# Optimization experiments

Hardware: AMD Instinct MI355X
Metric: run time of the kernel (lower is better)

The kernel has to match this reference:

```python
import jax, jax.numpy as jnp
import numpy as np

EMBED = 1024
HEADS = 16
HEAD_DIM = EMBED // HEADS
WINDOW = 256  # half-window = 128 on each side
B, S = 2, 2048


def setup_inputs() -> dict:
    key = jax.random.key(0)
    ks = jax.random.split(key, 9)
    std = 1.0 / np.sqrt(EMBED)
    def lin(k):
        kw, kb = jax.random.split(k)
        W = jax.random.uniform(kw, (EMBED, EMBED), jnp.float32, -std, std)
        b = jax.random.uniform(kb, (EMBED,), jnp.float32, -std, std)
        return W, b
    Wq, bq = lin(ks[0])
    Wk, bk = lin(ks[1])
    Wv, bv = lin(ks[2])
    Wo, bo = lin(ks[3])
    x = jax.random.normal(ks[4], (B, S, EMBED), jnp.float32)
    return {"x": x, "Wq": Wq, "bq": bq, "Wk": Wk, "bk": bk,
            "Wv": Wv, "bv": bv, "Wo": Wo, "bo": bo}


def reference(x, Wq, bq, Wk, bk, Wv, bv, Wo, bo):
    b, s, e = x.shape
    h, d = HEADS, HEAD_DIM
    # torch nn.Linear: y = x @ W.T + b
    def proj(W, bias):
        y = jnp.einsum('bse,fe->bsf', x, W) + bias
        return y.reshape(b, s, h, d).transpose(0, 2, 1, 3)  # [b,h,s,d]
    Q = proj(Wq, bq)
    K = proj(Wk, bk)
    V = proj(Wv, bv)
    # local mask: row i attends to cols [i - W//2, i + W//2] inclusive
    idx = jnp.arange(s)
    local_mask = jnp.abs(idx[:, None] - idx[None, :]) <= (WINDOW // 2)  # [s,s] bool
    scores = jnp.einsum('bhqd,bhkd->bhqk', Q, K) / jnp.sqrt(jnp.float32(d))
    scores = jnp.where(local_mask, scores, jnp.float32(-1e9))
    attn = jax.nn.softmax(scores, axis=-1)  # dropout is identity at eval
    out = jnp.einsum('bhqk,bhkd->bhqd', attn, V)
    out = out.transpose(0, 2, 1, 3).reshape(b, s, e)
    output = jnp.einsum('bse,fe->bsf', out, Wo) + bo
    return (output, attn)
```

## Files before the change

kernel.cpp:

```cpp
#include <hip/hip_runtime.h>
#include <hip/hip_bf16.h>
#include <stdint.h>

#define EMBED 1024
#define HEADS 16
#define HDIM 64
#define SEQ 2048
#define BATCH 2
#define MTOT (BATCH*SEQ)
#define KDIM EMBED
#define HALFW 128

typedef __attribute__((ext_vector_type(8))) short short8;
typedef __attribute__((ext_vector_type(4))) float floatx4;

__device__ __forceinline__ ushort f2bf(float f){
  uint32_t x = __float_as_uint(f);
  x += 0x7fffu + ((x >> 16) & 1u);
  return (ushort)(x >> 16);
}

__device__ __forceinline__ void gload16(const ushort* g, ushort* l){
  __builtin_amdgcn_global_load_lds(
      (__attribute__((address_space(1))) void*)(void*)g,
      (__attribute__((address_space(3))) void*)l, 16, 0, 0);
}

__global__ void cast_all(const float* __restrict__ x,  ushort* __restrict__ xb,
                         const float* __restrict__ Wq, const float* __restrict__ Wk,
                         const float* __restrict__ Wv, ushort* __restrict__ wqkv,
                         const float* __restrict__ Wo, ushort* __restrict__ wo)
{
  int bid = blockIdx.x;
  const float* src; ushort* dst; int base;
  if (bid < 4096){ src = x;  dst = xb;   base = bid; }
  else {
    int seg = (bid - 4096) >> 10;
    int sb  = (bid - 4096) & 1023;
    base = sb;
    if      (seg == 0){ src = Wq; dst = wqkv;           }
    else if (seg == 1){ src = Wk; dst = wqkv + 1048576; }
    else if (seg == 2){ src = Wv; dst = wqkv + 2097152; }
    else              { src = Wo; dst = wo;             }
  }
  int i = (base * 256 + threadIdx.x) * 4;
  float4 v = *reinterpret_cast<const float4*>(src + i);
  ushort4 o;
  o.x = f2bf(v.x); o.y = f2bf(v.y); o.z = f2bf(v.z); o.w = f2bf(v.w);
  *reinterpret_cast<ushort4*>(dst + i) = o;
}

__global__ __launch_bounds__(256) void gemm_qkv(
    const ushort* __restrict__ A, const ushort* __restrict__ Bw,
    const float* __restrict__ biasq, const float* __restrict__ biask, const float* __restrict__ biasv,
    ushort* __restrict__ Qo, ushort* __restrict__ Ko, ushort* __restrict__ Vo)
{
  constexpr int BM = 128, BN = 128, BK = 32;
  __shared__ __attribute__((aligned(16))) ushort As[BM*BK];
  __shared__ __attribute__((aligned(16))) ushort Bs[BN*BK];
  const int tid  = threadIdx.x;
  const int lane = tid & 63;
  const int wid  = tid >> 6;
  const int wr = wid >> 1, wc = wid & 1;
  const int m0 = blockIdx.x * BM;
  const int n0 = blockIdx.y * BN;

  floatx4 acc[4][4];
  #pragma unroll
  for (int i = 0; i < 4; ++i)
    #pragma unroll
    for (int j = 0; j < 4; ++j) acc[i][j] = (floatx4){0.f, 0.f, 0.f, 0.f};

  for (int kk = 0; kk < KDIM; kk += BK){
    if (kk) __syncthreads();
    #pragma unroll
    for (int rep = 0; rep < 2; ++rep){
      int cc = tid + rep * 256;
      int row = cc >> 2, off = (cc & 3) * 8;
      gload16(A  + (size_t)(m0 + row) * KDIM + kk + off, &As[cc * 8]);
      gload16(Bw + (size_t)(n0 + row) * KDIM + kk + off, &Bs[cc * 8]);
    }
    __syncthreads();

    short8 af[4], bfr[4];
    const int rsel = lane & 15, ksel = (lane >> 4) * 8;
    #pragma unroll
    for (int m = 0; m < 4; ++m)
      af[m] = *reinterpret_cast<const short8*>(&As[(wr*64 + m*16 + rsel) * BK + ksel]);
    #pragma unroll
    for (int n = 0; n < 4; ++n)
      bfr[n] = *reinterpret_cast<const short8*>(&Bs[(wc*64 + n*16 + rsel) * BK + ksel]);
    #pragma unroll
    for (int m = 0; m < 4; ++m)
      #pragma unroll
      for (int n = 0; n < 4; ++n)
        acc[m][n] = __builtin_amdgcn_mfma_f32_16x16x32_bf16(af[m], bfr[n], acc[m][n], 0, 0, 0);
  }

  const int which = n0 >> 10;
  const float* bias = (which == 0) ? biasq : ((which == 1) ? biask : biasv);
  ushort* dst = (which == 0) ? Qo : ((which == 1) ? Ko : Vo);
  const int nb = n0 & 1023;
  #pragma unroll
  for (int m = 0; m < 4; ++m)
    #pragma unroll
    for (int n = 0; n < 4; ++n)
      #pragma unroll
      for (int r = 0; r < 4; ++r){
        int mg = m0 + wr*64 + m*16 + (lane >> 4)*4 + r;
        int ng = nb + wc*64 + n*16 + (lane & 15);
        float v = acc[m][n][r] + bias[ng];
        int b = mg >> 11, s = mg & (SEQ - 1);
        int h = ng >> 6,  d = ng & 63;
        dst[(((size_t)(b*HEADS + h))*SEQ + s)*HDIM + d] = f2bf(v);
      }
}

__global__ __launch_bounds__(256) void transposeV(const ushort* __restrict__ V,
                                                  ushort* __restrict__ Vt)
{
  __shared__ ushort t[64][72];
  const int tid = threadIdx.x;
  const int bh = blockIdx.y;
  const int s0 = blockIdx.x * 64;
  #pragma unroll
  for (int it = 0; it < 2; ++it){
    int idx = it * 256 + tid;
    int row = idx >> 3, off = (idx & 7) * 8;
    *reinterpret_cast<uint4*>(&t[row][off]) =
        *reinterpret_cast<const uint4*>(V + ((size_t)bh * SEQ + s0 + row) * HDIM + off);
  }
  __syncthreads();
  #pragma unroll
  for (int it = 0; it < 2; ++it){
    int idx = it * 256 + tid;
    int d = idx >> 3, soff = (idx & 7) * 8;
    short8 v;
    #pragma unroll
    for (int e = 0; e < 8; ++e) v[e] = (short)t[soff + e][d];
    *reinterpret_cast<short8*>(Vt + ((size_t)bh * HDIM + d) * SEQ + s0 + soff) = v;
  }
}

__global__ __launch_bounds__(256) void gemm_out(
    const ushort* __restrict__ A, const ushort* __restrict__ Bw,
    const float* __restrict__ bias, float* __restrict__ Co)
{
  constexpr int BM = 128, BN = 128, BK = 32;
  __shared__ __attribute__((aligned(16))) ushort As[BM*BK];
  __shared__ __attribute__((aligned(16))) ushort Bs[BN*BK];
  const int tid  = threadIdx.x;
  const int lane = tid & 63;
  const int wid  = tid >> 6;
  const int wr = wid >> 1, wc = wid & 1;
  const int m0 = blockIdx.x * BM;
  const int n0 = blockIdx.y * BN;

  floatx4 acc[4][4];
  #pragma unroll
  for (int i = 0; i < 4; ++i)
    #pragma unroll
    for (int j = 0; j < 4; ++j) acc[i][j] = (floatx4){0.f, 0.f, 0.f, 0.f};

  for (int kk = 0; kk < KDIM; kk += BK){
    if (kk) __syncthreads();
    #pragma unroll
    for (int rep = 0; rep < 2; ++rep){
      int cc = tid + rep * 256;
      int row = cc >> 2, off = (cc & 3) * 8;
      gload16(A  + (size_t)(m0 + row) * KDIM + kk + off, &As[cc * 8]);
      gload16(Bw + (size_t)(n0 + row) * KDIM + kk + off, &Bs[cc * 8]);
    }
    __syncthreads();

    short8 af[4], bfr[4];
    const int rsel = lane & 15, ksel = (lane >> 4) * 8;
    #pragma unroll
    for (int m = 0; m < 4; ++m)
      af[m] = *reinterpret_cast<const short8*>(&As[(wr*64 + m*16 + rsel) * BK + ksel]);
    #pragma unroll
    for (int n = 0; n < 4; ++n)
      bfr[n] = *reinterpret_cast<const short8*>(&Bs[(wc*64 + n*16 + rsel) * BK + ksel]);
    #pragma unroll
    for (int m = 0; m < 4; ++m)
      #pragma unroll
      for (int n = 0; n < 4; ++n)
        acc[m][n] = __builtin_amdgcn_mfma_f32_16x16x32_bf16(af[m], bfr[n], acc[m][n], 0, 0, 0);
  }

  #pragma unroll
  for (int m = 0; m < 4; ++m)
    #pragma unroll
    for (int n = 0; n < 4; ++n)
      #pragma unroll
      for (int r = 0; r < 4; ++r){
        int mg = m0 + wr*64 + m*16 + (lane >> 4)*4 + r;
        int ng = n0 + wc*64 + n*16 + (lane & 15);
        Co[(size_t)mg * EMBED + ng] = acc[m][n][r] + bias[ng];
      }
}

__global__ __launch_bounds__(256) void attn_kernel(
    const ushort* __restrict__ Qb, const ushort* __restrict__ Kb, const ushort* __restrict__ Vt,
    float* __restrict__ attnp, ushort* __restrict__ ao)
{
  constexpr int TQ = 16;
  constexpr int SPAD = 292;
  constexpr int PPAD = 296;
  __shared__ __attribute__((aligned(16))) float  Ss[TQ][SPAD];
  __shared__ __attribute__((aligned(16))) ushort Pb[TQ][PPAD];
  __shared__ float rowinv[TQ];

  const int tid  = threadIdx.x;
  const int lane = tid & 63;
  const int w    = tid >> 6;
  const int l15  = lane & 15;
  const int lhi  = lane >> 4;
  const int qt = blockIdx.x;
  const int bh = blockIdx.y;
  const int q0 = qt * TQ;
  const int c0 = max(0, q0 - HALFW);
  const int c1 = min(SEQ, q0 + TQ + HALFW);
  const int nc = c1 - c0;
  const int ntiles = nc >> 4;
  const int nks = (nc + 31) >> 5;

  const ushort* Qrow = Qb + ((size_t)bh * SEQ + q0 + l15) * HDIM + lhi * 8;
  const short8 aq0 = *reinterpret_cast<const short8*>(Qrow);
  const short8 aq1 = *reinterpret_cast<const short8*>(Qrow + 32);

  for (int t = w; t < ntiles; t += 4){
    const ushort* Krow = Kb + ((size_t)bh * SEQ + c0 + t*16 + l15) * HDIM + lhi * 8;
    short8 bk0 = *reinterpret_cast<const short8*>(Krow);
    short8 bk1 = *reinterpret_cast<const short8*>(Krow + 32);
    floatx4 acc = (floatx4){0.f, 0.f, 0.f, 0.f};
    acc = __builtin_amdgcn_mfma_f32_16x16x32_bf16(aq0, bk0, acc, 0, 0, 0);
    acc = __builtin_amdgcn_mfma_f32_16x16x32_bf16(aq1, bk1, acc, 0, 0, 0);
    const int c = c0 + t*16 + l15;
    #pragma unroll
    for (int r = 0; r < 4; ++r){
      int q = q0 + lhi*4 + r;
      float s = (c < q - HALFW || c > q + HALFW) ? -1e30f : acc[r] * 0.125f;
      Ss[lhi*4 + r][t*16 + l15] = s;
    }
  }
  __syncthreads();

  const int r  = tid >> 4;
  const int lc = tid & 15;
  float mx = -1e30f;
  for (int j = lc; j < nc; j += 16) mx = fmaxf(mx, Ss[r][j]);
  #pragma unroll
  for (int o = 1; o < 16; o <<= 1) mx = fmaxf(mx, __shfl_xor(mx, o, 64));
  float sum = 0.f;
  for (int j = lc; j < nc; j += 16){
    float p = __expf(Ss[r][j] - mx);
    Ss[r][j] = p;
    Pb[r][j] = f2bf(p);
    sum += p;
  }
  for (int j = nc + lc; j < nks * 32; j += 16) Pb[r][j] = 0;
  #pragma unroll
  for (int o = 1; o < 16; o <<= 1) sum += __shfl_xor(sum, o, 64);
  if (lc == 0) rowinv[r] = 1.f / sum;
  __syncthreads();

  const int jz0 = c0 >> 2, jz1 = c1 >> 2;
  const floatx4 zero4 = (floatx4){0.f, 0.f, 0.f, 0.f};
  for (int rr = 0; rr < TQ; ++rr){
    const float inv = rowinv[rr];
    floatx4* dst = reinterpret_cast<floatx4*>(attnp + ((size_t)bh * SEQ + (q0 + rr)) * SEQ);
    #pragma unroll
    for (int it = 0; it < SEQ / 4 / 256; ++it){
      int j4 = it * 256 + tid;
      floatx4 v = zero4;
      if (j4 >= jz0 && j4 < jz1){
        floatx4 p = *reinterpret_cast<const floatx4*>(&Ss[rr][j4 * 4 - c0]);
        v = (floatx4){p[0] * inv, p[1] * inv, p[2] * inv, p[3] * inv};
      }
      __builtin_nontemporal_store(v, &dst[j4]);
    }
  }

  floatx4 oacc = (floatx4){0.f, 0.f, 0.f, 0.f};
  const ushort* Vrow = Vt + ((size_t)bh * HDIM + w*16 + l15) * SEQ + c0 + lhi * 8;
  for (int ks = 0; ks < nks; ++ks){
    short8 ap = *reinterpret_cast<const short8*>(&Pb[l15][ks*32 + lhi*8]);
    short8 bv = *reinterpret_cast<const short8*>(Vrow + ks*32);
    oacc = __builtin_amdgcn_mfma_f32_16x16x32_bf16(ap, bv, oacc, 0, 0, 0);
  }
  const int b = bh >> 4, h = bh & 15;
  #pragma unroll
  for (int rr = 0; rr < 4; ++rr){
    int q = q0 + lhi*4 + rr;
    float val = oacc[rr] * rowinv[lhi*4 + rr];
    ao[((size_t)(b * SEQ + q)) * EMBED + h * HDIM + w*16 + l15] = f2bf(val);
  }
}

extern "C" void kernel_launch(void* const* d_in, const int* in_sizes, int n_in,
                              void* d_out, int out_size, void* d_ws, size_t ws_size,
                              hipStream_t stream)
{
  const float* x  = (const float*)d_in[0];
  const float* Wq = (const float*)d_in[1];
  const float* bq = (const float*)d_in[2];
  const float* Wk = (const float*)d_in[3];
  const float* bk = (const float*)d_in[4];
  const float* Wv = (const float*)d_in[5];
  const float* bv = (const float*)d_in[6];
  const float* Wo = (const float*)d_in[7];
  const float* bo = (const float*)d_in[8];

  char* ws = (char*)d_ws;
  ushort* xb   = (ushort*)(ws);
  ushort* wqkv = (ushort*)(ws + 8388608);
  ushort* wo   = (ushort*)(ws + 14680064);
  ushort* Qb   = (ushort*)(ws + 16777216);
  ushort* Kb   = (ushort*)(ws + 25165824);
  ushort* Vb   = (ushort*)(ws + 33554432);
  ushort* ao   = (ushort*)(ws + 41943040);
  ushort* Vt   = (ushort*)(ws);

  float* outp  = (float*)d_out;
  float* attnp = outp + (size_t)MTOT * EMBED;

  cast_all<<<8192, 256, 0, stream>>>(x, xb, Wq, Wk, Wv, wqkv, Wo, wo);
  gemm_qkv<<<dim3(32, 24), 256, 0, stream>>>(xb, wqkv, bq, bk, bv, Qb, Kb, Vb);
  transposeV<<<dim3(32, 32), 256, 0, stream>>>(Vb, Vt);
  attn_kernel<<<dim3(128, 32), 256, 0, stream>>>(Qb, Kb, Vt, attnp, ao);
  gemm_out<<<dim3(32, 8), 256, 0, stream>>>(ao, wo, bo, outp);
}
```

Baseline: 183.3 us.

## Double-buffer LDS tiles and swizzle block order in projection GEMMs

Both projection GEMMs now use two LDS buffers, prefetching the next K tile via global_load_lds while MFMAs consume the current one, with one barrier per iteration. The grid is flattened to 1D and block indices are remapped so consecutive blocks on the same XCD share tiles for better cache reuse. The cost is doubled shared memory per block, which may reduce occupancy.

```diff
diff --git a/kernel.cpp b/kernel.cpp
--- a/kernel.cpp
+++ b/kernel.cpp
@@ -56,14 +56,25 @@
     ushort* __restrict__ Qo, ushort* __restrict__ Ko, ushort* __restrict__ Vo)
 {
   constexpr int BM = 128, BN = 128, BK = 32;
-  __shared__ __attribute__((aligned(16))) ushort As[BM*BK];
-  __shared__ __attribute__((aligned(16))) ushort Bs[BN*BK];
+  __shared__ __attribute__((aligned(16))) ushort As[2][BM*BK];
+  __shared__ __attribute__((aligned(16))) ushort Bs[2][BN*BK];
   const int tid  = threadIdx.x;
   const int lane = tid & 63;
   const int wid  = tid >> 6;
   const int wr = wid >> 1, wc = wid & 1;
-  const int m0 = blockIdx.x * BM;
-  const int n0 = blockIdx.y * BN;
+
+  const int bid = blockIdx.x;
+  const int swz = (bid & 7) * 96 + (bid >> 3);
+  const int m0 = (swz & 31) * BM;
+  const int n0 = (swz >> 5) * BN;
+
+  const int cc0 = tid, cc1 = tid + 256;
+  const int row0 = cc0 >> 2, off0 = (cc0 & 3) * 8;
+  const int row1 = cc1 >> 2, off1 = (cc1 & 3) * 8;
+  const ushort* A0 = A  + (size_t)(m0 + row0) * KDIM + off0;
+  const ushort* A1 = A  + (size_t)(m0 + row1) * KDIM + off1;
+  const ushort* B0 = Bw + (size_t)(n0 + row0) * KDIM + off0;
+  const ushort* B1 = Bw + (size_t)(n0 + row1) * KDIM + off1;
 
   floatx4 acc[4][4];
   #pragma unroll
@@ -71,30 +82,36 @@
     #pragma unroll
     for (int j = 0; j < 4; ++j) acc[i][j] = (floatx4){0.f, 0.f, 0.f, 0.f};
 
+  const int rsel = lane & 15, ksel = (lane >> 4) * 8;
+
+  gload16(A0, &As[0][cc0 * 8]);
+  gload16(B0, &Bs[0][cc0 * 8]);
+  gload16(A1, &As[0][cc1 * 8]);
+  gload16(B1, &Bs[0][cc1 * 8]);
+  __syncthreads();
+
+  int cur = 0;
   for (int kk = 0; kk < KDIM; kk += BK){
-    if (kk) __syncthreads();
-    #pragma unroll
-    for (int rep = 0; rep < 2; ++rep){
-      int cc = tid + rep * 256;
-      int row = cc >> 2, off = (cc & 3) * 8;
-      gload16(A  + (size_t)(m0 + row) * KDIM + kk + off, &As[cc * 8]);
-      gload16(Bw + (size_t)(n0 + row) * KDIM + kk + off, &Bs[cc * 8]);
+    if (kk + BK < KDIM){
+      gload16(A0 + kk + BK, &As[cur ^ 1][cc0 * 8]);
+      gload16(B0 + kk + BK, &Bs[cur ^ 1][cc0 * 8]);
+      gload16(A1 + kk + BK, &As[cur ^ 1][cc1 * 8]);
+      gload16(B1 + kk + BK, &Bs[cur ^ 1][cc1 * 8]);
     }
-    __syncthreads();
-
     short8 af[4], bfr[4];
-    const int rsel = lane & 15, ksel = (lane >> 4) * 8;
     #pragma unroll
     for (int m = 0; m < 4; ++m)
-      af[m] = *reinterpret_cast<const short8*>(&As[(wr*64 + m*16 + rsel) * BK + ksel]);
+      af[m] = *reinterpret_cast<const short8*>(&As[cur][(wr*64 + m*16 + rsel) * BK + ksel]);
     #pragma unroll
     for (int n = 0; n < 4; ++n)
-      bfr[n] = *reinterpret_cast<const short8*>(&Bs[(wc*64 + n*16 + rsel) * BK + ksel]);
+      bfr[n] = *reinterpret_cast<const short8*>(&Bs[cur][(wc*64 + n*16 + rsel) * BK + ksel]);
     #pragma unroll
     for (int m = 0; m < 4; ++m)
       #pragma unroll
       for (int n = 0; n < 4; ++n)
         acc[m][n] = __builtin_amdgcn_mfma_f32_16x16x32_bf16(af[m], bfr[n], acc[m][n], 0, 0, 0);
+    __syncthreads();
+    cur ^= 1;
   }
 
   const int which = n0 >> 10;
@@ -147,14 +164,25 @@
     const float* __restrict__ bias, float* __restrict__ Co)
 {
   constexpr int BM = 128, BN = 128, BK = 32;
-  __shared__ __attribute__((aligned(16))) ushort As[BM*BK];
-  __shared__ __attribute__((aligned(16))) ushort Bs[BN*BK];
+  __shared__ __attribute__((aligned(16))) ushort As[2][BM*BK];
+  __shared__ __attribute__((aligned(16))) ushort Bs[2][BN*BK];
   const int tid  = threadIdx.x;
   const int lane = tid & 63;
   const int wid  = tid >> 6;
   const int wr = wid >> 1, wc = wid & 1;
-  const int m0 = blockIdx.x * BM;
-  const int n0 = blockIdx.y * BN;
+
+  const int bid = blockIdx.x;
+  const int swz = (bid & 7) * 32 + (bid >> 3);
+  const int m0 = (swz & 31) * BM;
+  const int n0 = (swz >> 5) * BN;
+
+  const int cc0 = tid, cc1 = tid + 256;
+  const int row0 = cc0 >> 2, off0 = (cc0 & 3) * 8;
+  const int row1 = cc1 >> 2, off1 = (cc1 & 3) * 8;
+  const ushort* A0 = A  + (size_t)(m0 + row0) * KDIM + off0;
+  const ushort* A1 = A  + (size_t)(m0 + row1) * KDIM + off1;
+  const ushort* B0 = Bw + (size_t)(n0 + row0) * KDIM + off0;
+  const ushort* B1 = Bw + (size_t)(n0 + row1) * KDIM + off1;
 
   floatx4 acc[4][4];
   #pragma unroll
@@ -162,30 +190,36 @@
     #pragma unroll
     for (int j = 0; j < 4; ++j) acc[i][j] = (floatx4){0.f, 0.f, 0.f, 0.f};
 
+  const int rsel = lane & 15, ksel = (lane >> 4) * 8;
+
+  gload16(A0, &As[0][cc0 * 8]);
+  gload16(B0, &Bs[0][cc0 * 8]);
+  gload16(A1, &As[0][cc1 * 8]);
+  gload16(B1, &Bs[0][cc1 * 8]);
+  __syncthreads();
+
+  int cur = 0;
   for (int kk = 0; kk < KDIM; kk += BK){
-    if (kk) __syncthreads();
-    #pragma unroll
-    for (int rep = 0; rep < 2; ++rep){
-      int cc = tid + rep * 256;
-      int row = cc >> 2, off = (cc & 3) * 8;
-      gload16(A  + (size_t)(m0 + row) * KDIM + kk + off, &As[cc * 8]);
-      gload16(Bw + (size_t)(n0 + row) * KDIM + kk + off, &Bs[cc * 8]);
+    if (kk + BK < KDIM){
+      gload16(A0 + kk + BK, &As[cur ^ 1][cc0 * 8]);
+      gload16(B0 + kk + BK, &Bs[cur ^ 1][cc0 * 8]);
+      gload16(A1 + kk + BK, &As[cur ^ 1][cc1 * 8]);
+      gload16(B1 + kk + BK, &Bs[cur ^ 1][cc1 * 8]);
     }
-    __syncthreads();
-
     short8 af[4], bfr[4];
-    const int rsel = lane & 15, ksel = (lane >> 4) * 8;
     #pragma unroll
     for (int m = 0; m < 4; ++m)
-      af[m] = *reinterpret_cast<const short8*>(&As[(wr*64 + m*16 + rsel) * BK + ksel]);
+      af[m] = *reinterpret_cast<const short8*>(&As[cur][(wr*64 + m*16 + rsel) * BK + ksel]);
     #pragma unroll
     for (int n = 0; n < 4; ++n)
-      bfr[n] = *reinterpret_cast<const short8*>(&Bs[(wc*64 + n*16 + rsel) * BK + ksel]);
+      bfr[n] = *reinterpret_cast<const short8*>(&Bs[cur][(wc*64 + n*16 + rsel) * BK + ksel]);
     #pragma unroll
     for (int m = 0; m < 4; ++m)
       #pragma unroll
       for (int n = 0; n < 4; ++n)
         acc[m][n] = __builtin_amdgcn_mfma_f32_16x16x32_bf16(af[m], bfr[n], acc[m][n], 0, 0, 0);
+    __syncthreads();
+    cur ^= 1;
   }
 
   #pragma unroll
@@ -326,8 +360,8 @@
   float* attnp = outp + (size_t)MTOT * EMBED;
 
   cast_all<<<8192, 256, 0, stream>>>(x, xb, Wq, Wk, Wv, wqkv, Wo, wo);
-  gemm_qkv<<<dim3(32, 24), 256, 0, stream>>>(xb, wqkv, bq, bk, bv, Qb, Kb, Vb);
+  gemm_qkv<<<768, 256, 0, stream>>>(xb, wqkv, bq, bk, bv, Qb, Kb, Vb);
   transposeV<<<dim3(32, 32), 256, 0, stream>>>(Vb, Vt);
   attn_kernel<<<dim3(128, 32), 256, 0, stream>>>(Qb, Kb, Vt, attnp, ao);
-  gemm_out<<<dim3(32, 8), 256, 0, stream>>>(ao, wo, bo, outp);
-}
+  gemm_out<<<256, 256, 0, stream>>>(ao, wo, bo, outp);
+}
```

After: 182.0 us. No clear change (-0.7%).
